# Performance work log

Hardware: AMD Instinct MI355X
Metric: run time of the kernel (lower is better)

The kernel has to match this reference:

```python
import jax, jax.numpy as jnp
import numpy as np

N = 50000        # nodes
E = 400000       # edges (avg degree 8)
F_IN = 128       # num_features
HID = 64         # hidden_channels
H = 4            # num_heads
D = HID // H     # headc = 16
C = 16           # num_classes
K_HOPS = 3
ALPHA = 0.1
CST = 1e-5


def setup_inputs() -> dict:
    key = jax.random.key(0)
    ks = jax.random.split(key, 16)
    s = 0.05
    x = jax.random.normal(ks[0], (N, F_IN), dtype=jnp.float32)
    edge_index = jax.random.randint(ks[1], (2, E), 0, N, dtype=jnp.int64)
    Wi = jax.random.normal(ks[2], (F_IN, HID), dtype=jnp.float32) * s
    bi = jnp.zeros((HID,), dtype=jnp.float32)
    Wq = jax.random.normal(ks[3], (HID, H * D), dtype=jnp.float32) * s
    bq = jnp.zeros((H * D,), dtype=jnp.float32)
    Wk = jax.random.normal(ks[4], (HID, H * D), dtype=jnp.float32) * s
    bk = jnp.zeros((H * D,), dtype=jnp.float32)
    Wv = jax.random.normal(ks[5], (HID, H * C), dtype=jnp.float32) * s
    bv = jnp.zeros((H * C,), dtype=jnp.float32)
    Wo = jax.random.normal(ks[6], (H * C, C), dtype=jnp.float32) * s
    bo = jnp.zeros((C,), dtype=jnp.float32)
    # hopwise/temp init as in the torch module (ind_gamma=True, gamma_softmax=True)
    hw = ALPHA * (1.0 - ALPHA) ** np.arange(K_HOPS + 1)
    hw[-1] = (1.0 - ALPHA) ** K_HOPS
    hopwise = jnp.asarray(hw, dtype=jnp.float32)
    temp = jax.random.uniform(ks[7], (H, K_HOPS + 1), dtype=jnp.float32)
    return {"x": x, "edge_index": edge_index, "Wi": Wi, "bi": bi, "Wq": Wq,
            "bq": bq, "Wk": Wk, "bk": bk, "Wv": Wv, "bv": bv, "Wo": Wo,
            "bo": bo, "hopwise": hopwise, "temp": temp}


def reference(x, edge_index, Wi, bi, Wq, bq, Wk, bk, Wv, bv, Wo, bo, hopwise, temp):
    # dropout p=0 (inference); input transform + relu
    h = jax.nn.relu(x @ Wi + bi)                       # (N, HID)
    Q = (1.0 + jax.nn.elu(h @ Wq + bq)).reshape(N, H, D)
    Kt = (1.0 + jax.nn.elu(h @ Wk + bk)).reshape(N, H, D)
    V = (h @ Wv + bv).reshape(N, H, C)
    M = jnp.einsum('nhi,nhj->nhij', Kt, V)             # (N, H, D, C)
    hidden = V * temp[:, 0][None, :, None]             # hop-0 term
    # NB: torch F.softmax(temp, dim=-2) normalizes over the HEAD axis
    layerwise = jax.nn.softmax(temp, axis=0)           # (H, K+1)
    src, dst = edge_index[0], edge_index[1]
    for hop in range(K_HOPS):
        M = jax.ops.segment_sum(M[src], dst, num_segments=N)
        Kt = jax.ops.segment_sum(Kt[src], dst, num_segments=N)
        Hm = jnp.einsum('nhi,nhij->nhj', Q, M)         # (N, H, C)
        den = jnp.einsum('nhi,nhi->nh', Q, Kt)[..., None] + CST
        gamma = hopwise[hop + 1] * layerwise[:, hop + 1][:, None]  # (H, 1)
        hidden = hidden + gamma * (Hm / den)
    # multi_concat=True path
    out = hidden.reshape(N, H * C) @ Wo + bo           # (N, C)
    return out
```

## Files before the change

kernel.cpp:

```cpp
#include <hip/hip_runtime.h>
#include <math.h>

#define F_IN 128
#define HID  64
#define NH   4
#define DD   16
#define CC   16
#define CSTE 1e-5f

typedef _Float16 h2     __attribute__((ext_vector_type(2)));
typedef float    f2     __attribute__((ext_vector_type(2)));
typedef short    short8 __attribute__((ext_vector_type(8)));
typedef float    f4v    __attribute__((ext_vector_type(4)));

#define WIT_LD 136
#define W2T_LD 72
#define H_LD   72

__device__ __forceinline__ unsigned short bf16r(float f) {
    unsigned int u = __builtin_bit_cast(unsigned int, f);
    unsigned int r = (u + 0x7FFFu + ((u >> 16) & 1u)) >> 16;
    return (unsigned short)r;
}

__device__ __forceinline__ float fp8_to_f32(unsigned int b) {
    f2 v = __builtin_amdgcn_cvt_pk_f32_fp8((int)b, false);
    return v.x;
}
__device__ __forceinline__ unsigned char f32_to_fp8(float f) {
    int w = __builtin_amdgcn_cvt_pk_fp8_f32(f, f, 0, false);
    return (unsigned char)(w & 0xff);
}

#if __has_builtin(__builtin_amdgcn_cvt_scalef32_pk_f32_fp4) && __has_builtin(__builtin_amdgcn_cvt_scalef32_pk_fp4_f32)
#define HAS_FP4 1
#endif

#ifndef HAS_FP4
__device__ __forceinline__ float fp4_dec1(unsigned int n) {
    unsigned int e = (n >> 1) & 3u, m = n & 1u;
    float mag = (e == 0) ? 0.5f * (float)m
                         : (float)(1u << (e - 1)) * (1.0f + 0.5f * (float)m);
    return (n & 8u) ? -mag : mag;
}
__device__ __forceinline__ unsigned int fp4_enc1(float f) {
    unsigned int s = (f < 0.f) ? 8u : 0u;
    float a = fabsf(f);
    unsigned int m;
    if      (a < 0.25f) m = 0u;
    else if (a < 0.75f) m = 1u;
    else if (a < 1.25f) m = 2u;
    else if (a < 1.75f) m = 3u;
    else if (a < 2.5f)  m = 4u;
    else if (a < 3.5f)  m = 5u;
    else if (a < 5.0f)  m = 6u;
    else                m = 7u;
    return s | m;
}
#endif

__device__ __forceinline__ void fp4x16_dec(uint2 w, float* v) {
#ifdef HAS_FP4
    f2 r;
    r = __builtin_amdgcn_cvt_scalef32_pk_f32_fp4(w.x, 1.0f, 0); v[0]  = r.x; v[1]  = r.y;
    r = __builtin_amdgcn_cvt_scalef32_pk_f32_fp4(w.x, 1.0f, 1); v[2]  = r.x; v[3]  = r.y;
    r = __builtin_amdgcn_cvt_scalef32_pk_f32_fp4(w.x, 1.0f, 2); v[4]  = r.x; v[5]  = r.y;
    r = __builtin_amdgcn_cvt_scalef32_pk_f32_fp4(w.x, 1.0f, 3); v[6]  = r.x; v[7]  = r.y;
    r = __builtin_amdgcn_cvt_scalef32_pk_f32_fp4(w.y, 1.0f, 0); v[8]  = r.x; v[9]  = r.y;
    r = __builtin_amdgcn_cvt_scalef32_pk_f32_fp4(w.y, 1.0f, 1); v[10] = r.x; v[11] = r.y;
    r = __builtin_amdgcn_cvt_scalef32_pk_f32_fp4(w.y, 1.0f, 2); v[12] = r.x; v[13] = r.y;
    r = __builtin_amdgcn_cvt_scalef32_pk_f32_fp4(w.y, 1.0f, 3); v[14] = r.x; v[15] = r.y;
#else
    #pragma unroll
    for (int j = 0; j < 8; ++j) {
        v[j]     = fp4_dec1((w.x >> (4 * j)) & 0xFu);
        v[8 + j] = fp4_dec1((w.y >> (4 * j)) & 0xFu);
    }
#endif
}

__device__ __forceinline__ uint2 fp4x16_enc(const float* v) {
#ifdef HAS_FP4
    unsigned int a = 0u, b = 0u;
    a = __builtin_amdgcn_cvt_scalef32_pk_fp4_f32(a, v[0],  v[1],  1.0f, 0);
    a = __builtin_amdgcn_cvt_scalef32_pk_fp4_f32(a, v[2],  v[3],  1.0f, 1);
    a = __builtin_amdgcn_cvt_scalef32_pk_fp4_f32(a, v[4],  v[5],  1.0f, 2);
    a = __builtin_amdgcn_cvt_scalef32_pk_fp4_f32(a, v[6],  v[7],  1.0f, 3);
    b = __builtin_amdgcn_cvt_scalef32_pk_fp4_f32(b, v[8],  v[9],  1.0f, 0);
    b = __builtin_amdgcn_cvt_scalef32_pk_fp4_f32(b, v[10], v[11], 1.0f, 1);
    b = __builtin_amdgcn_cvt_scalef32_pk_fp4_f32(b, v[12], v[13], 1.0f, 2);
    b = __builtin_amdgcn_cvt_scalef32_pk_fp4_f32(b, v[14], v[15], 1.0f, 3);
    return {a, b};
#else
    unsigned int a = 0u, b = 0u;
    #pragma unroll
    for (int j = 0; j < 8; ++j) {
        a |= fp4_enc1(v[j])     << (4 * j);
        b |= fp4_enc1(v[8 + j]) << (4 * j);
    }
    return {a, b};
#endif
}

__device__ __forceinline__ void store_m_row(
    uint2* __restrict__ Mout, unsigned short* __restrict__ SKout,
    int node, int lane, const float* u, float kacc)
{
    float rm = 0.f;
    #pragma unroll
    for (int j = 0; j < 16; ++j) rm = fmaxf(rm, fabsf(u[j]));
    unsigned char s8 = f32_to_fp8(rm * (1.0f / 6.0f));
    float se = fp8_to_f32((unsigned int)s8);
    float invs = (se > 0.f) ? (1.0f / se) : 0.f;
    float tq[16];
    #pragma unroll
    for (int j = 0; j < 16; ++j) tq[j] = u[j] * invs;
    Mout[(size_t)node * 64 + lane] = fp4x16_enc(tq);
    SKout[(size_t)node * 64 + lane] =
        (unsigned short)((unsigned short)s8 | ((unsigned short)f32_to_fp8(kacc) << 8));
}

__device__ __forceinline__ float gamma_for(const float* __restrict__ temp,
                                           const float* __restrict__ hopwise,
                                           int h, int hop) {
    float t0 = temp[0 * 4 + hop], t1 = temp[1 * 4 + hop];
    float t2 = temp[2 * 4 + hop], t3 = temp[3 * 4 + hop];
    float mx = fmaxf(fmaxf(t0, t1), fmaxf(t2, t3));
    float e0 = __expf(t0 - mx), e1 = __expf(t1 - mx);
    float e2 = __expf(t2 - mx), e3 = __expf(t3 - mx);
    float ssum = e0 + e1 + e2 + e3;
    float eh = (h == 0) ? e0 : (h == 1) ? e1 : (h == 2) ? e2 : e3;
    return hopwise[hop] * eh / ssum;
}

__global__ void count_kernel(const int* __restrict__ ei, int* __restrict__ deg, int E) {
    int e = blockIdx.x * blockDim.x + threadIdx.x;
    if (e < E) atomicAdd(&deg[ei[E + e]], 1);
}

__global__ __launch_bounds__(1024) void scan_a(const int* __restrict__ deg,
                                               int* __restrict__ offsets,
                                               int* __restrict__ bsum, int N) {
    __shared__ int wsum[16], woff[16];
    int lane = threadIdx.x & 63, w = threadIdx.x >> 6;
    int i0 = blockIdx.x * 4096 + (int)threadIdx.x * 4;
    int d0 = (i0 + 0 < N) ? deg[i0 + 0] : 0;
    int d1 = (i0 + 1 < N) ? deg[i0 + 1] : 0;
    int d2 = (i0 + 2 < N) ? deg[i0 + 2] : 0;
    int d3 = (i0 + 3 < N) ? deg[i0 + 3] : 0;
    int tsum = d0 + d1 + d2 + d3;
    int incl = tsum;
    #pragma unroll
    for (int m = 1; m < 64; m <<= 1) {
        int t = __shfl_up(incl, m, 64);
        if (lane >= m) incl += t;
    }
    if (lane == 63) wsum[w] = incl;
    __syncthreads();
    if (threadIdx.x == 0) {
        int r = 0;
        for (int k = 0; k < 16; ++k) { int t = wsum[k]; woff[k] = r; r += t; }
        bsum[blockIdx.x] = r;
    }
    __syncthreads();
    int excl = woff[w] + incl - tsum;
    if (i0 + 0 < N) offsets[i0 + 0] = excl;
    if (i0 + 1 < N) offsets[i0 + 1] = excl + d0;
    if (i0 + 2 < N) offsets[i0 + 2] = excl + d0 + d1;
    if (i0 + 3 < N) offsets[i0 + 3] = excl + d0 + d1 + d2;
}

__global__ void scan_c(int* __restrict__ offsets, const int* __restrict__ bsum,
                       int nb, int N) {
    int i = blockIdx.x * blockDim.x + threadIdx.x;
    if (i < N) {
        int bkt = i >> 12;
        int base = 0;
        for (int b = 0; b < bkt; ++b) base += bsum[b];
        offsets[i] += base;
    }
    if (i == 0) {
        int tot = 0;
        for (int b = 0; b < nb; ++b) tot += bsum[b];
        offsets[N] = tot;
    }
}

__global__ void scatter_kernel(const int* __restrict__ ei, const int* __restrict__ offsets,
                               int* __restrict__ cursor, int* __restrict__ csr, int E) {
    int e = blockIdx.x * blockDim.x + threadIdx.x;
    if (e < E) {
        int src = ei[e];
        int dst = ei[E + e];
        int pos = atomicAdd(&cursor[dst], 1);
        csr[offsets[dst] + pos] = src;
    }
}

__global__ __launch_bounds__(256) void qkv_mfma(
    const float* __restrict__ x,
    const float* __restrict__ Wi, const float* __restrict__ bi,
    const float* __restrict__ Wq, const float* __restrict__ bq,
    const float* __restrict__ Wk, const float* __restrict__ bk,
    const float* __restrict__ Wv, const float* __restrict__ bv,
    const float* __restrict__ temp,
    float* __restrict__ Q, unsigned char* __restrict__ K0,
    _Float16* __restrict__ Vh, float* __restrict__ hidden, int N)
{
    __shared__ unsigned short wit[64 * WIT_LD];
    __shared__ unsigned short w2t[192 * W2T_LD];
    __shared__ unsigned short hlds[64 * H_LD];
    int t = threadIdx.x;
    #pragma unroll
    for (int i = 0; i < 32; ++i) {
        int g = t + i * 256;
        wit[(g & 63) * WIT_LD + (g >> 6)] = bf16r(Wi[g]);
    }
    #pragma unroll
    for (int i = 0; i < 16; ++i) {
        int g = t + i * 256;
        int k = g >> 6, n = g & 63;
        w2t[(n      ) * W2T_LD + k] = bf16r(Wq[g]);
        w2t[(n +  64) * W2T_LD + k] = bf16r(Wk[g]);
        w2t[(n + 128) * W2T_LD + k] = bf16r(Wv[g]);
    }
    __syncthreads();

    int lane = t & 63, w = t >> 6;
    int p = lane & 15, quad = lane >> 4;
    int mbase = blockIdx.x * 64 + w * 16;

    short8 afrag[4];
    {
        int node = mbase + p;
        if (node >= N) node = N - 1;
        const float* xr = x + (size_t)node * F_IN + quad * 8;
        #pragma unroll
        for (int ks = 0; ks < 4; ++ks) {
            float4 a0 = *(const float4*)(xr + ks * 32);
            float4 a1 = *(const float4*)(xr + ks * 32 + 4);
            short8 f;
            f[0] = bf16r(a0.x); f[1] = bf16r(a0.y); f[2] = bf16r(a0.z); f[3] = bf16r(a0.w);
            f[4] = bf16r(a1.x); f[5] = bf16r(a1.y); f[6] = bf16r(a1.z); f[7] = bf16r(a1.w);
            afrag[ks] = f;
        }
    }
    #pragma unroll
    for (int nt = 0; nt < 4; ++nt) {
        f4v acc = {0.f, 0.f, 0.f, 0.f};
        #pragma unroll
        for (int ks = 0; ks < 4; ++ks) {
            short8 b = *(const short8*)&wit[(nt * 16 + p) * WIT_LD + ks * 32 + quad * 8];
            acc = __builtin_amdgcn_mfma_f32_16x16x32_bf16(afrag[ks], b, acc, 0, 0, 0);
        }
        float bb = bi[nt * 16 + p];
        #pragma unroll
        for (int r = 0; r < 4; ++r) {
            float hv = fmaxf(acc[r] + bb, 0.f);
            hlds[(w * 16 + quad * 4 + r) * H_LD + nt * 16 + p] = bf16r(hv);
        }
    }
    __syncthreads();

    short8 ha0 = *(const short8*)&hlds[(w * 16 + p) * H_LD + quad * 8];
    short8 ha1 = *(const short8*)&hlds[(w * 16 + p) * H_LD + 32 + quad * 8];
    int node_r = mbase + quad * 4;
    #pragma unroll
    for (int nt = 0; nt < 12; ++nt) {
        f4v acc = {0.f, 0.f, 0.f, 0.f};
        short8 b0 = *(const short8*)&w2t[(nt * 16 + p) * W2T_LD + quad * 8];
        short8 b1 = *(const short8*)&w2t[(nt * 16 + p) * W2T_LD + 32 + quad * 8];
        acc = __builtin_amdgcn_mfma_f32_16x16x32_bf16(ha0, b0, acc, 0, 0, 0);
        acc = __builtin_amdgcn_mfma_f32_16x16x32_bf16(ha1, b1, acc, 0, 0, 0);
        int col = nt * 16 + p;
        #pragma unroll
        for (int r = 0; r < 4; ++r) {
            int node = node_r + r;
            if (node >= N) continue;
            float v = acc[r];
            if (col < 64) {
                v += bq[col];
                Q[(size_t)node * 64 + col] = (v > 0.f) ? (1.f + v) : __expf(v);
            } else if (col < 128) {
                int c = col - 64;
                v += bk[c];
                float kv = (v > 0.f) ? (1.f + v) : __expf(v);
                K0[(size_t)node * 64 + c] = f32_to_fp8(kv);
            } else {
                int c = col - 128;
                v += bv[c];
                Vh[(size_t)node * 64 + c] = (_Float16)v;
                hidden[(size_t)node * 64 + c] = v * temp[(c >> 4) * 4];
            }
        }
    }
}


__device__ __forceinline__ void hop_epilogue(
    float* u, float qd, float kacc, float gh,
    float* __restrict__ hidden, int node, int lane)
{
    int p = lane & 15;
    #pragma unroll
    for (int j = 0; j < 16; ++j) u[j] *= qd;
    #pragma unroll
    for (int k = 0; k < 4; ++k) {
        const int m = 1 << k;
        bool bit = (p >> k) & 1;
        const int n = 8 >> k;
        #pragma unroll
        for (int j = 0; j < n; ++j) {
            float give = bit ? u[2 * j]     : u[2 * j + 1];
            float keep = bit ? u[2 * j + 1] : u[2 * j];
            float got  = __shfl_xor(give, m, 64);
            u[j] = keep + got;
        }
    }
    float kq = qd * kacc;
    kq += __shfl_xor(kq, 1, 64);
    kq += __shfl_xor(kq, 2, 64);
    kq += __shfl_xor(kq, 4, 64);
    kq += __shfl_xor(kq, 8, 64);
    float g = gh / (kq + CSTE);
    hidden[(size_t)node * 64 + lane] += g * u[0];
}

__global__ __launch_bounds__(256) void hop1_all(
    const float* __restrict__ Q, const unsigned char* __restrict__ K0,
    const _Float16* __restrict__ Vh,
    const int* __restrict__ offsets, const int* __restrict__ csr,
    const float* __restrict__ temp, const float* __restrict__ hopwise,
    uint2* __restrict__ M1, unsigned short* __restrict__ SK1,
    float* __restrict__ hidden, int N)
{
    int lane = threadIdx.x & 63;
    int node = blockIdx.x * 4 + (threadIdx.x >> 6);
    if (node >= N) return;
    int h = lane >> 4;
    float gh = gamma_for(temp, hopwise, h, 1);
    h2 u16[8];
    #pragma unroll
    for (int j = 0; j < 8; ++j) u16[j] = h2{(_Float16)0.f, (_Float16)0.f};
    float kacc = 0.f;
    int beg = offsets[node], end = offsets[node + 1];
    int t = beg;
    for (; t + 1 < end; t += 2) {
        int s0 = csr[t], s1 = csr[t + 1];
        const uint4* v0p = (const uint4*)(Vh + (size_t)s0 * 64 + h * 16);
        const uint4* v1p = (const uint4*)(Vh + (size_t)s1 * 64 + h * 16);
        uint4 a0 = v0p[0], a1 = v0p[1];
        uint4 b0 = v1p[0], b1 = v1p[1];
        float k0 = fp8_to_f32(K0[(size_t)s0 * 64 + lane]);
        float k1 = fp8_to_f32(K0[(size_t)s1 * 64 + lane]);
        kacc += k0 + k1;
        _Float16 k0h = (_Float16)k0, k1h = (_Float16)k1;
        h2 k02 = {k0h, k0h}, k12 = {k1h, k1h};
        const unsigned int aw[8] = {a0.x, a0.y, a0.z, a0.w, a1.x, a1.y, a1.z, a1.w};
        const unsigned int bw[8] = {b0.x, b0.y, b0.z, b0.w, b1.x, b1.y, b1.z, b1.w};
        #pragma unroll
        for (int j = 0; j < 8; ++j) {
            u16[j] += k02 * __builtin_bit_cast(h2, aw[j]);
            u16[j] += k12 * __builtin_bit_cast(h2, bw[j]);
        }
    }
    for (; t < end; ++t) {
        int s = csr[t];
        const uint4* vp = (const uint4*)(Vh + (size_t)s * 64 + h * 16);
        uint4 a0 = vp[0], a1 = vp[1];
        float kk = fp8_to_f32(K0[(size_t)s * 64 + lane]);
        kacc += kk;
        _Float16 kh = (_Float16)kk;
        h2 k2 = {kh, kh};
        const unsigned int aw[8] = {a0.x, a0.y, a0.z, a0.w, a1.x, a1.y, a1.z, a1.w};
        #pragma unroll
        for (int j = 0; j < 8; ++j)
            u16[j] += k2 * __builtin_bit_cast(h2, aw[j]);
    }
    float u[16];
    #pragma unroll
    for (int j = 0; j < 8; ++j) { u[2 * j] = (float)u16[j].x; u[2 * j + 1] = (float)u16[j].y; }
    store_m_row(M1, SK1, node, lane, u, kacc);
    float qd = Q[(size_t)node * 64 + lane];
    hop_epilogue(u, qd, kacc, gh, hidden, node, lane);
}

template<bool STORE>
__global__ __launch_bounds__(256) void hop23_all(
    const float* __restrict__ Q, const uint2* __restrict__ Mprev,
    const unsigned short* __restrict__ SKprev,
    const int* __restrict__ offsets, const int* __restrict__ csr,
    const float* __restrict__ temp, const float* __restrict__ hopwise,
    uint2* __restrict__ Mnext, unsigned short* __restrict__ SKnext,
    float* __restrict__ hidden, int N, int hop)
{
    int lane = threadIdx.x & 63;
    int node = blockIdx.x * 4 + (threadIdx.x >> 6);
    if (node >= N) return;
    float gh = gamma_for(temp, hopwise, lane >> 4, hop);
    const uint2* Mb = Mprev + lane;
    const unsigned short* SKb = SKprev + lane;
    float u[16];
    #pragma unroll
    for (int j = 0; j < 16; ++j) u[j] = 0.f;
    float kacc = 0.f;
    int beg = offsets[node], end = offsets[node + 1];
    int t = beg;
    for (; t + 3 < end; t += 4) {
        int s0 = csr[t], s1 = csr[t + 1], s2 = csr[t + 2], s3 = csr[t + 3];
        uint2 w0 = Mb[(size_t)s0 * 64];
        uint2 w1 = Mb[(size_t)s1 * 64];
        uint2 w2 = Mb[(size_t)s2 * 64];
        uint2 w3 = Mb[(size_t)s3 * 64];
        unsigned int q0 = SKb[(size_t)s0 * 64];
        unsigned int q1 = SKb[(size_t)s1 * 64];
        unsigned int q2 = SKb[(size_t)s2 * 64];
        unsigned int q3 = SKb[(size_t)s3 * 64];
        kacc += (fp8_to_f32(q0 >> 8) + fp8_to_f32(q1 >> 8))
              + (fp8_to_f32(q2 >> 8) + fp8_to_f32(q3 >> 8));
        float v[16];
        float s;
        s = fp8_to_f32(q0 & 0xffu); fp4x16_dec(w0, v);
        #pragma unroll
        for (int j = 0; j < 16; ++j) u[j] = fmaf(s, v[j], u[j]);
        s = fp8_to_f32(q1 & 0xffu); fp4x16_dec(w1, v);
        #pragma unroll
        for (int j = 0; j < 16; ++j) u[j] = fmaf(s, v[j], u[j]);
        s = fp8_to_f32(q2 & 0xffu); fp4x16_dec(w2, v);
        #pragma unroll
        for (int j = 0; j < 16; ++j) u[j] = fmaf(s, v[j], u[j]);
        s = fp8_to_f32(q3 & 0xffu); fp4x16_dec(w3, v);
        #pragma unroll
        for (int j = 0; j < 16; ++j) u[j] = fmaf(s, v[j], u[j]);
    }
    for (; t < end; ++t) {
        int sn = csr[t];
        uint2 w = Mb[(size_t)sn * 64];
        unsigned int q = SKb[(size_t)sn * 64];
        kacc += fp8_to_f32(q >> 8);
        float v[16];
        float s = fp8_to_f32(q & 0xffu);
        fp4x16_dec(w, v);
        #pragma unroll
        for (int j = 0; j < 16; ++j) u[j] = fmaf(s, v[j], u[j]);
    }
    if (STORE) store_m_row(Mnext, SKnext, node, lane, u, kacc);
    float qd = Q[(size_t)node * 64 + lane];
    hop_epilogue(u, qd, kacc, gh, hidden, node, lane);
}

__global__ __launch_bounds__(256) void out_kernel(
    const float* __restrict__ hidden, const float* __restrict__ Wo,
    const float* __restrict__ bo, float* __restrict__ out, int N)
{
    __shared__ float wo[HID * CC];
    for (int i = threadIdx.x; i < HID * CC; i += 256) wo[i] = Wo[i];
    __syncthreads();
    int idx = blockIdx.x * 256 + threadIdx.x;
    int n = idx >> 4, c = idx & 15;
    if (n >= N) return;
    float acc = bo[c];
    const float4* hp4 = (const float4*)(hidden + (size_t)n * HID);
    #pragma unroll
    for (int j4 = 0; j4 < 16; ++j4) {
        float4 hv = hp4[j4];
        acc += hv.x * wo[(4 * j4 + 0) * CC + c] + hv.y * wo[(4 * j4 + 1) * CC + c]
             + hv.z * wo[(4 * j4 + 2) * CC + c] + hv.w * wo[(4 * j4 + 3) * CC + c];
    }
    out[(size_t)n * CC + c] = acc;
}

extern "C" void kernel_launch(void* const* d_in, const int* in_sizes, int n_in,
                              void* d_out, int out_size, void* d_ws, size_t ws_size,
                              hipStream_t stream) {
    const float* x       = (const float*)d_in[0];
    const int*   ei      = (const int*)  d_in[1];
    const float* Wi      = (const float*)d_in[2];
    const float* bi      = (const float*)d_in[3];
    const float* Wq      = (const float*)d_in[4];
    const float* bq      = (const float*)d_in[5];
    const float* Wk      = (const float*)d_in[6];
    const float* bk      = (const float*)d_in[7];
    const float* Wv      = (const float*)d_in[8];
    const float* bv      = (const float*)d_in[9];
    const float* Wo      = (const float*)d_in[10];
    const float* bo      = (const float*)d_in[11];
    const float* hopwise = (const float*)d_in[12];
    const float* temp    = (const float*)d_in[13];

    const int N = in_sizes[0] / F_IN;
    const int E = in_sizes[1] / 2;

    char* ws = (char*)d_ws;
    size_t off = 0;
    auto take = [&](size_t bytes) -> char* {
        char* p = ws + off;
        off += (bytes + 255) & ~(size_t)255;
        return p;
    };
    float*          Q      = (float*)take((size_t)N * 64 * 4);
    _Float16*       Vh     = (_Float16*)take((size_t)N * 64 * 2);
    float*          hidden = (float*)take((size_t)N * 64 * 4);
    unsigned char*  K0     = (unsigned char*)take((size_t)N * 64);
    unsigned short* SK1    = (unsigned short*)take((size_t)N * 64 * 2);
    unsigned short* SK2    = (unsigned short*)take((size_t)N * 64 * 2);
    int*            degcur = (int*)take((size_t)2 * N * 4);
    int*            offs   = (int*)take((size_t)(N + 1) * 4);
    int*            csr    = (int*)take((size_t)E * 4);
    int             nb     = (N + 4095) / 4096;
    int*            bsum   = (int*)take((size_t)nb * 4);
    uint2*          M1     = (uint2*)take((size_t)N * 512);
    uint2*          M2     = (uint2*)take((size_t)N * 512);

    int* deg    = degcur;
    int* cursor = degcur + N;

    hipMemsetAsync(degcur, 0, (size_t)2 * N * 4, stream);

    int eb = (E + 255) / 256;
    count_kernel<<<eb, 256, 0, stream>>>(ei, deg, E);
    scan_a<<<nb, 1024, 0, stream>>>(deg, offs, bsum, N);
    scan_c<<<(N + 255) / 256, 256, 0, stream>>>(offs, bsum, nb, N);
    scatter_kernel<<<eb, 256, 0, stream>>>(ei, offs, cursor, csr, E);

    int qb = (N + 63) / 64;
    qkv_mfma<<<qb, 256, 0, stream>>>(x, Wi, bi, Wq, bq, Wk, bk, Wv, bv,
                                     temp, Q, K0, Vh, hidden, N);

    int nb4 = (N + 3) / 4;
    hop1_all<<<nb4, 256, 0, stream>>>(Q, K0, Vh, offs, csr, temp, hopwise,
                                      M1, SK1, hidden, N);
    hop23_all<true ><<<nb4, 256, 0, stream>>>(Q, M1, SK1, offs, csr, temp, hopwise,
                                              M2, SK2, hidden, N, 2);
    hop23_all<false><<<nb4, 256, 0, stream>>>(Q, M2, SK2, offs, csr, temp, hopwise,
                                              (uint2*)nullptr, (unsigned short*)nullptr,
                                              hidden, N, 3);

    int ob = (N * CC + 255) / 256;
    out_kernel<<<ob, 256, 0, stream>>>(hidden, Wo, bo, (float*)d_out, N);
}
```

Measured before the change: 320.1 us.

## Fuse degree count into QKV kernel and output projection into final hop

```diff
diff --git a/kernel.cpp b/kernel.cpp
--- a/kernel.cpp
+++ b/kernel.cpp
@@ -27,16 +27,14 @@
     f2 v = __builtin_amdgcn_cvt_pk_f32_fp8((int)b, false);
     return v.x;
 }
+__device__ __forceinline__ f2 fp8x2_to_f32(unsigned int w) {
+    return __builtin_amdgcn_cvt_pk_f32_fp8((int)w, false);
+}
 __device__ __forceinline__ unsigned char f32_to_fp8(float f) {
     int w = __builtin_amdgcn_cvt_pk_fp8_f32(f, f, 0, false);
     return (unsigned char)(w & 0xff);
 }
 
-#if __has_builtin(__builtin_amdgcn_cvt_scalef32_pk_f32_fp4) && __has_builtin(__builtin_amdgcn_cvt_scalef32_pk_fp4_f32)
-#define HAS_FP4 1
-#endif
-
-#ifndef HAS_FP4
 __device__ __forceinline__ float fp4_dec1(unsigned int n) {
     unsigned int e = (n >> 1) & 3u, m = n & 1u;
     float mag = (e == 0) ? 0.5f * (float)m
@@ -57,6 +55,9 @@
     else                m = 7u;
     return s | m;
 }
+
+#if __has_builtin(__builtin_amdgcn_cvt_scalef32_pk_f32_fp4) && __has_builtin(__builtin_amdgcn_cvt_scalef32_pk_fp4_f32)
+#define HAS_FP4 1
 #endif
 
 __device__ __forceinline__ void fp4x16_dec(uint2 w, float* v) {
@@ -133,9 +134,29 @@
     return hopwise[hop] * eh / ssum;
 }
 
-__global__ void count_kernel(const int* __restrict__ ei, int* __restrict__ deg, int E) {
-    int e = blockIdx.x * blockDim.x + threadIdx.x;
-    if (e < E) atomicAdd(&deg[ei[E + e]], 1);
+__device__ __forceinline__ void reduce_scatter16(float* u, int p) {
+    #pragma unroll
+    for (int k = 0; k < 4; ++k) {
+        const int m = 1 << k;
+        bool bit = (p >> k) & 1;
+        const int n = 8 >> k;
+        #pragma unroll
+        for (int j = 0; j < n; ++j) {
+            float give = bit ? u[2 * j]     : u[2 * j + 1];
+            float keep = bit ? u[2 * j + 1] : u[2 * j];
+            float got  = __shfl_xor(give, m, 64);
+            u[j] = keep + got;
+        }
+    }
+}
+
+__device__ __forceinline__ float den16(float qd, float kacc) {
+    float kq = qd * kacc;
+    kq += __shfl_xor(kq, 1, 64);
+    kq += __shfl_xor(kq, 2, 64);
+    kq += __shfl_xor(kq, 4, 64);
+    kq += __shfl_xor(kq, 8, 64);
+    return kq + CSTE;
 }
 
 __global__ __launch_bounds__(1024) void scan_a(const int* __restrict__ deg,
@@ -197,7 +218,7 @@
     }
 }
 
-__global__ __launch_bounds__(256) void qkv_mfma(
+__global__ __launch_bounds__(256) void qkv_count(
     const float* __restrict__ x,
     const float* __restrict__ Wi, const float* __restrict__ bi,
     const float* __restrict__ Wq, const float* __restrict__ bq,
@@ -205,11 +226,18 @@
     const float* __restrict__ Wv, const float* __restrict__ bv,
     const float* __restrict__ temp,
     float* __restrict__ Q, unsigned char* __restrict__ K0,
-    _Float16* __restrict__ Vh, float* __restrict__ hidden, int N)
+    _Float16* __restrict__ Vh, float* __restrict__ hidden,
+    const int* __restrict__ ei, int* __restrict__ deg,
+    int E, int qb, int N)
 {
     __shared__ unsigned short wit[64 * WIT_LD];
     __shared__ unsigned short w2t[192 * W2T_LD];
     __shared__ unsigned short hlds[64 * H_LD];
+    if ((int)blockIdx.x >= qb) {
+        int e = ((int)blockIdx.x - qb) * 256 + (int)threadIdx.x;
+        if (e < E) atomicAdd(&deg[ei[E + e]], 1);
+        return;
+    }
     int t = threadIdx.x;
     #pragma unroll
     for (int i = 0; i < 32; ++i) {
@@ -297,35 +325,6 @@
 }
 
 
-__device__ __forceinline__ void hop_epilogue(
-    float* u, float qd, float kacc, float gh,
-    float* __restrict__ hidden, int node, int lane)
-{
-    int p = lane & 15;
-    #pragma unroll
-    for (int j = 0; j < 16; ++j) u[j] *= qd;
-    #pragma unroll
-    for (int k = 0; k < 4; ++k) {
-        const int m = 1 << k;
-        bool bit = (p >> k) & 1;
-        const int n = 8 >> k;
-        #pragma unroll
-        for (int j = 0; j < n; ++j) {
-            float give = bit ? u[2 * j]     : u[2 * j + 1];
-            float keep = bit ? u[2 * j + 1] : u[2 * j];
-            float got  = __shfl_xor(give, m, 64);
-            u[j] = keep + got;
-        }
-    }
-    float kq = qd * kacc;
-    kq += __shfl_xor(kq, 1, 64);
-    kq += __shfl_xor(kq, 2, 64);
-    kq += __shfl_xor(kq, 4, 64);
-    kq += __shfl_xor(kq, 8, 64);
-    float g = gh / (kq + CSTE);
-    hidden[(size_t)node * 64 + lane] += g * u[0];
-}
-
 __global__ __launch_bounds__(256) void hop1_all(
     const float* __restrict__ Q, const unsigned char* __restrict__ K0,
     const _Float16* __restrict__ Vh,
@@ -382,22 +381,25 @@
     for (int j = 0; j < 8; ++j) { u[2 * j] = (float)u16[j].x; u[2 * j + 1] = (float)u16[j].y; }
     store_m_row(M1, SK1, node, lane, u, kacc);
     float qd = Q[(size_t)node * 64 + lane];
-    hop_epilogue(u, qd, kacc, gh, hidden, node, lane);
-}
-
-template<bool STORE>
-__global__ __launch_bounds__(256) void hop23_all(
+    #pragma unroll
+    for (int j = 0; j < 16; ++j) u[j] *= qd;
+    reduce_scatter16(u, lane & 15);
+    float g = gh / den16(qd, kacc);
+    hidden[(size_t)node * 64 + lane] += g * u[0];
+}
+
+__global__ __launch_bounds__(256) void hop2_all(
     const float* __restrict__ Q, const uint2* __restrict__ Mprev,
     const unsigned short* __restrict__ SKprev,
     const int* __restrict__ offsets, const int* __restrict__ csr,
     const float* __restrict__ temp, const float* __restrict__ hopwise,
     uint2* __restrict__ Mnext, unsigned short* __restrict__ SKnext,
-    float* __restrict__ hidden, int N, int hop)
+    float* __restrict__ hidden, int N)
 {
     int lane = threadIdx.x & 63;
     int node = blockIdx.x * 4 + (threadIdx.x >> 6);
     if (node >= N) return;
-    float gh = gamma_for(temp, hopwise, lane >> 4, hop);
+    float gh = gamma_for(temp, hopwise, lane >> 4, 2);
     const uint2* Mb = Mprev + lane;
     const unsigned short* SKb = SKprev + lane;
     float u[16];
@@ -412,62 +414,123 @@
         uint2 w1 = Mb[(size_t)s1 * 64];
         uint2 w2 = Mb[(size_t)s2 * 64];
         uint2 w3 = Mb[(size_t)s3 * 64];
-        unsigned int q0 = SKb[(size_t)s0 * 64];
-        unsigned int q1 = SKb[(size_t)s1 * 64];
-        unsigned int q2 = SKb[(size_t)s2 * 64];
-        unsigned int q3 = SKb[(size_t)s3 * 64];
-        kacc += (fp8_to_f32(q0 >> 8) + fp8_to_f32(q1 >> 8))
-              + (fp8_to_f32(q2 >> 8) + fp8_to_f32(q3 >> 8));
+        f2 sk0 = fp8x2_to_f32(SKb[(size_t)s0 * 64]);
+        f2 sk1 = fp8x2_to_f32(SKb[(size_t)s1 * 64]);
+        f2 sk2 = fp8x2_to_f32(SKb[(size_t)s2 * 64]);
+        f2 sk3 = fp8x2_to_f32(SKb[(size_t)s3 * 64]);
+        kacc += (sk0.y + sk1.y) + (sk2.y + sk3.y);
         float v[16];
-        float s;
-        s = fp8_to_f32(q0 & 0xffu); fp4x16_dec(w0, v);
-        #pragma unroll
-        for (int j = 0; j < 16; ++j) u[j] = fmaf(s, v[j], u[j]);
-        s = fp8_to_f32(q1 & 0xffu); fp4x16_dec(w1, v);
-        #pragma unroll
-        for (int j = 0; j < 16; ++j) u[j] = fmaf(s, v[j], u[j]);
-        s = fp8_to_f32(q2 & 0xffu); fp4x16_dec(w2, v);
-        #pragma unroll
-        for (int j = 0; j < 16; ++j) u[j] = fmaf(s, v[j], u[j]);
-        s = fp8_to_f32(q3 & 0xffu); fp4x16_dec(w3, v);
-        #pragma unroll
-        for (int j = 0; j < 16; ++j) u[j] = fmaf(s, v[j], u[j]);
+        fp4x16_dec(w0, v);
+        #pragma unroll
+        for (int j = 0; j < 16; ++j) u[j] = fmaf(sk0.x, v[j], u[j]);
+        fp4x16_dec(w1, v);
+        #pragma unroll
+        for (int j = 0; j < 16; ++j) u[j] = fmaf(sk1.x, v[j], u[j]);
+        fp4x16_dec(w2, v);
+        #pragma unroll
+        for (int j = 0; j < 16; ++j) u[j] = fmaf(sk2.x, v[j], u[j]);
+        fp4x16_dec(w3, v);
+        #pragma unroll
+        for (int j = 0; j < 16; ++j) u[j] = fmaf(sk3.x, v[j], u[j]);
     }
     for (; t < end; ++t) {
         int sn = csr[t];
         uint2 w = Mb[(size_t)sn * 64];
-        unsigned int q = SKb[(size_t)sn * 64];
-        kacc += fp8_to_f32(q >> 8);
+        f2 sk = fp8x2_to_f32(SKb[(size_t)sn * 64]);
+        kacc += sk.y;
         float v[16];
-        float s = fp8_to_f32(q & 0xffu);
         fp4x16_dec(w, v);
         #pragma unroll
-        for (int j = 0; j < 16; ++j) u[j] = fmaf(s, v[j], u[j]);
-    }
-    if (STORE) store_m_row(Mnext, SKnext, node, lane, u, kacc);
+        for (int j = 0; j < 16; ++j) u[j] = fmaf(sk.x, v[j], u[j]);
+    }
+    store_m_row(Mnext, SKnext, node, lane, u, kacc);
     float qd = Q[(size_t)node * 64 + lane];
-    hop_epilogue(u, qd, kacc, gh, hidden, node, lane);
-}
-
-__global__ __launch_bounds__(256) void out_kernel(
+    #pragma unroll
+    for (int j = 0; j < 16; ++j) u[j] *= qd;
+    reduce_scatter16(u, lane & 15);
+    float g = gh / den16(qd, kacc);
+    hidden[(size_t)node * 64 + lane] += g * u[0];
+}
+
+__global__ __launch_bounds__(256) void hop3_out(
+    const float* __restrict__ Q, const uint2* __restrict__ Mprev,
+    const unsigned short* __restrict__ SKprev,
+    const int* __restrict__ offsets, const int* __restrict__ csr,
+    const float* __restrict__ temp, const float* __restrict__ hopwise,
     const float* __restrict__ hidden, const float* __restrict__ Wo,
     const float* __restrict__ bo, float* __restrict__ out, int N)
 {
-    __shared__ float wo[HID * CC];
-    for (int i = threadIdx.x; i < HID * CC; i += 256) wo[i] = Wo[i];
-    __syncthreads();
-    int idx = blockIdx.x * 256 + threadIdx.x;
-    int n = idx >> 4, c = idx & 15;
-    if (n >= N) return;
-    float acc = bo[c];
-    const float4* hp4 = (const float4*)(hidden + (size_t)n * HID);
-    #pragma unroll
-    for (int j4 = 0; j4 < 16; ++j4) {
-        float4 hv = hp4[j4];
-        acc += hv.x * wo[(4 * j4 + 0) * CC + c] + hv.y * wo[(4 * j4 + 1) * CC + c]
-             + hv.z * wo[(4 * j4 + 2) * CC + c] + hv.w * wo[(4 * j4 + 3) * CC + c];
-    }
-    out[(size_t)n * CC + c] = acc;
+    int lane = threadIdx.x & 63;
+    int node = blockIdx.x * 4 + (threadIdx.x >> 6);
+    if (node >= N) return;
+    float gh = gamma_for(temp, hopwise, lane >> 4, 3);
+    float wor[16];
+    {
+        const float4* wp = (const float4*)(Wo + lane * 16);
+        float4 a = wp[0], b = wp[1], c = wp[2], d = wp[3];
+        wor[0] = a.x; wor[1] = a.y; wor[2]  = a.z; wor[3]  = a.w;
+        wor[4] = b.x; wor[5] = b.y; wor[6]  = b.z; wor[7]  = b.w;
+        wor[8] = c.x; wor[9] = c.y; wor[10] = c.z; wor[11] = c.w;
+        wor[12] = d.x; wor[13] = d.y; wor[14] = d.z; wor[15] = d.w;
+    }
+    float bov = bo[lane & 15];
+    const uint2* Mb = Mprev + lane;
+    const unsigned short* SKb = SKprev + lane;
+    float u[16];
+    #pragma unroll
+    for (int j = 0; j < 16; ++j) u[j] = 0.f;
+    float kacc = 0.f;
+    int beg = offsets[node], end = offsets[node + 1];
+    int t = beg;
+    for (; t + 3 < end; t += 4) {
+        int s0 = csr[t], s1 = csr[t + 1], s2 = csr[t + 2], s3 = csr[t + 3];
+        uint2 w0 = Mb[(size_t)s0 * 64];
+        uint2 w1 = Mb[(size_t)s1 * 64];
+        uint2 w2 = Mb[(size_t)s2 * 64];
+        uint2 w3 = Mb[(size_t)s3 * 64];
+        f2 sk0 = fp8x2_to_f32(SKb[(size_t)s0 * 64]);
+        f2 sk1 = fp8x2_to_f32(SKb[(size_t)s1 * 64]);
+        f2 sk2 = fp8x2_to_f32(SKb[(size_t)s2 * 64]);
+        f2 sk3 = fp8x2_to_f32(SKb[(size_t)s3 * 64]);
+        kacc += (sk0.y + sk1.y) + (sk2.y + sk3.y);
+        float v[16];
+        fp4x16_dec(w0, v);
+        #pragma unroll
+        for (int j = 0; j < 16; ++j) u[j] = fmaf(sk0.x, v[j], u[j]);
+        fp4x16_dec(w1, v);
+        #pragma unroll
+        for (int j = 0; j < 16; ++j) u[j] = fmaf(sk1.x, v[j], u[j]);
+        fp4x16_dec(w2, v);
+        #pragma unroll
+        for (int j = 0; j < 16; ++j) u[j] = fmaf(sk2.x, v[j], u[j]);
+        fp4x16_dec(w3, v);
+        #pragma unroll
+        for (int j = 0; j < 16; ++j) u[j] = fmaf(sk3.x, v[j], u[j]);
+    }
+    for (; t < end; ++t) {
+        int sn = csr[t];
+        uint2 w = Mb[(size_t)sn * 64];
+        f2 sk = fp8x2_to_f32(SKb[(size_t)sn * 64]);
+        kacc += sk.y;
+        float v[16];
+        fp4x16_dec(w, v);
+        #pragma unroll
+        for (int j = 0; j < 16; ++j) u[j] = fmaf(sk.x, v[j], u[j]);
+    }
+    float qd = Q[(size_t)node * 64 + lane];
+    #pragma unroll
+    for (int j = 0; j < 16; ++j) u[j] *= qd;
+    reduce_scatter16(u, lane & 15);
+    float g = gh / den16(qd, kacc);
+    float hval = hidden[(size_t)node * 64 + lane] + g * u[0];
+    float o[16];
+    #pragma unroll
+    for (int c = 0; c < 16; ++c) o[c] = hval * wor[c];
+    reduce_scatter16(o, lane & 15);
+    float tot = o[0];
+    tot += __shfl_xor(tot, 16, 64);
+    tot += __shfl_xor(tot, 32, 64);
+    if (lane < 16) out[(size_t)node * 16 + lane] = tot + bov;
 }
 
 extern "C" void kernel_launch(void* const* d_in, const int* in_sizes, int n_in,
@@ -518,24 +581,19 @@
     hipMemsetAsync(degcur, 0, (size_t)2 * N * 4, stream);
 
     int eb = (E + 255) / 256;
-    count_kernel<<<eb, 256, 0, stream>>>(ei, deg, E);
+    int qb = (N + 63) / 64;
+    qkv_count<<<qb + eb, 256, 0, stream>>>(x, Wi, bi, Wq, bq, Wk, bk, Wv, bv,
+                                           temp, Q, K0, Vh, hidden,
+                                           ei, deg, E, qb, N);
     scan_a<<<nb, 1024, 0, stream>>>(deg, offs, bsum, N);
     scan_c<<<(N + 255) / 256, 256, 0, stream>>>(offs, bsum, nb, N);
     scatter_kernel<<<eb, 256, 0, stream>>>(ei, offs, cursor, csr, E);
 
-    int qb = (N + 63) / 64;
-    qkv_mfma<<<qb, 256, 0, stream>>>(x, Wi, bi, Wq, bq, Wk, bk, Wv, bv,
-                                     temp, Q, K0, Vh, hidden, N);
-
     int nb4 = (N + 3) / 4;
     hop1_all<<<nb4, 256, 0, stream>>>(Q, K0, Vh, offs, csr, temp, hopwise,
                                       M1, SK1, hidden, N);
-    hop23_all<true ><<<nb4, 256, 0, stream>>>(Q, M1, SK1, offs, csr, temp, hopwise,
-                                              M2, SK2, hidden, N, 2);
-    hop23_all<false><<<nb4, 256, 0, stream>>>(Q, M2, SK2, offs, csr, temp, hopwise,
-                                              (uint2*)nullptr, (unsigned short*)nullptr,
-                                              hidden, N, 3);
-
-    int ob = (N * CC + 255) / 256;
-    out_kernel<<<ob, 256, 0, stream>>>(hidden, Wo, bo, (float*)d_out, N);
-}
+    hop2_all<<<nb4, 256, 0, stream>>>(Q, M1, SK1, offs, csr, temp, hopwise,
+                                      M2, SK2, hidden, N);
+    hop3_out<<<nb4, 256, 0, stream>>>(Q, M2, SK2, offs, csr, temp, hopwise,
+                                      hidden, Wo, bo, (float*)d_out, N);
+}
```

Result: no change. 325.2 us (+1.6%).
